# Kernel optimization log

Measured on AMD Instinct MI355X. Metric: run time of the kernel, lower is better.

Reference implementation:

```python
import jax, jax.numpy as jnp
import numpy as np

B, L, C, R = 2, 1024, 64, 32
RV, DQK, H, NSINK = 32, 64, 8, 4


def setup_inputs() -> dict:
    key = jax.random.key(0)
    ks = jax.random.split(key, 10)
    s_in = 1.0 / np.sqrt(C * R)
    s_r = 1.0 / np.sqrt(R)
    s_rv = 1.0 / np.sqrt(RV)
    return {
        "x": jax.random.normal(ks[0], (B, L, C, R), jnp.float32),
        "Wq": jax.random.normal(ks[1], (C * R, H * DQK), jnp.float32) * s_in,
        "bq": jax.random.normal(ks[2], (H * DQK,), jnp.float32) * s_in,
        "Wk": jax.random.normal(ks[3], (C * R, DQK), jnp.float32) * s_in,
        "bk": jax.random.normal(ks[4], (DQK,), jnp.float32) * s_in,
        "Wv": jax.random.normal(ks[5], (C, R, RV), jnp.float32) * s_r,
        "bv": jax.random.normal(ks[6], (C, RV), jnp.float32) * s_r,
        "Wo": jax.random.normal(ks[7], (C, RV, R), jnp.float32) * s_rv,
        "bo": jax.random.normal(ks[8], (C, R), jnp.float32) * s_rv,
        "sink_q": jax.random.normal(ks[9], (H, NSINK, DQK), jnp.float32),
    }


def reference(x, Wq, bq, Wk, bk, Wv, bv, Wo, bo, sink_q):
    b, l, c, r = x.shape
    h, d_qk = H, DQK
    scale = 1.0 / np.sqrt(d_qk)

    x_flat = x.reshape(b, l, c * r)
    q = (x_flat @ Wq + bq).reshape(b, l, h, d_qk)          # (B,L,H,D)
    k = x_flat @ Wk + bk                                    # (B,L,D) shared MQA key

    # fp32 softmax over time, as in the original
    logits = (jnp.einsum('blhd,bsd->bhls', q, k).astype(jnp.float32) * scale)
    attn = jax.nn.softmax(logits, axis=-1).astype(x.dtype)  # (B,H,L,S)

    # per-channel value projection (B,L,C,RV)
    v = jnp.einsum('blcr,cro->blco', x, Wv) + bv

    # AV with extra channel axis, fused with head-mean (same math as
    # einsum('bhls,bscv->bhlcv').mean(1))
    y = jnp.einsum('bhls,bscv->blcv', attn, v) / h          # (B,L,C,RV)

    # sink-query branch: learned queries attend over time, mean over (H, S)
    logits_s = (jnp.einsum('hsd,bld->bhsl', sink_q, k).astype(jnp.float32) * scale)
    attn_s = jax.nn.softmax(logits_s, axis=-1).astype(x.dtype)  # (B,H,S,L)
    y_sink = jnp.einsum('bhsl,blcv->bcv', attn_s, v) / (h * NSINK)
    y = y + y_sink[:, None]                                 # broadcast over L

    # per-channel output projection + residual
    y = jnp.einsum('blcv,cvr->blcr', y, Wo) + bo
    return x + y
```

## Files before the change

kernel.cpp:

```cpp
#include <hip/hip_runtime.h>
#include <hip/hip_bf16.h>
#include <math.h>


typedef __attribute__((ext_vector_type(8))) short short8;
typedef __attribute__((ext_vector_type(4))) short short4v;
typedef __attribute__((ext_vector_type(4))) float float4v;

__device__ __forceinline__ short f2b(float f) {
    __hip_bfloat16 h = __float2bfloat16(f);
    return __builtin_bit_cast(short, h);
}
__device__ __forceinline__ float b2f(short s) {
    unsigned u = ((unsigned)(unsigned short)s) << 16;
    return __builtin_bit_cast(float, u);
}

__global__ __launch_bounds__(256) void convert_w_kernel(
    const float* __restrict__ Wq, const float* __restrict__ Wk,
    short* __restrict__ Wt)
{
    const int n0 = blockIdx.x * 64;
    const int k0 = blockIdx.y * 64;
    const int tid = threadIdx.x;
    __shared__ float ts[64][65];
    for (int i = tid; i < 4096; i += 256) {
        int kk = i >> 6, nn = i & 63;
        int n = n0 + nn, k = k0 + kk;
        float v = (n < 512) ? Wq[(long)k * 512 + n] : Wk[(long)k * 64 + (n - 512)];
        ts[kk][nn] = v;
    }
    __syncthreads();
    for (int i = tid; i < 4096; i += 256) {
        int nn = i >> 6, kk = i & 63;
        Wt[(long)(n0 + nn) * 2048 + k0 + kk] = f2b(ts[kk][nn]);
    }
}

__global__ __launch_bounds__(256) void vproj_kernel(
    const float* __restrict__ x, const float* __restrict__ Wv,
    const float* __restrict__ bv, short* __restrict__ vt,
    short* __restrict__ xb)
{
    const int c = blockIdx.x;
    const int chunk = blockIdx.y;
    const int b = chunk >> 4;
    const int l0 = (chunk & 15) * 64;
    const int tid = threadIdx.x;
    __shared__ float Wc[32][33];
    __shared__ float xs[64][33];
    for (int i = tid; i < 1024; i += 256)
        Wc[i >> 5][i & 31] = Wv[(c * 32 + (i >> 5)) * 32 + (i & 31)];
    for (int i = tid; i < 2048; i += 256) {
        int s = i >> 5, r = i & 31;
        long gi = ((long)(b << 10) + l0 + s) * 2048 + c * 32 + r;
        float v = x[gi];
        xs[s][r] = v;
        xb[gi] = f2b(v);
    }
    __syncthreads();
    const int s = tid & 63;
    const int og = tid >> 6;
    #pragma unroll
    for (int oi = 0; oi < 8; ++oi) {
        int o = og * 8 + oi;
        float acc = bv[c * 32 + o];
        #pragma unroll
        for (int r = 0; r < 32; ++r) acc += xs[s][r] * Wc[r][o];
        vt[(long)b * (2048 * 1024) + (long)(c * 32 + o) * 1024 + l0 + s] = f2b(acc);
    }
}

__global__ __launch_bounds__(256) void qkproj_kernel(
    const short* __restrict__ xb, const short* __restrict__ Wt,
    float* __restrict__ qkpart)
{
    __shared__ short As[64][72];
    __shared__ short Bs[64][72];

    const int tid = threadIdx.x;
    const int wave = tid >> 6;
    const int lane = tid & 63;
    const int wm = wave >> 1, wn = wave & 1;
    const int m15 = lane & 15;
    const int quad = lane >> 4;
    const int row0 = blockIdx.y * 64;
    const int col0 = blockIdx.x * 64;
    const int kbase = blockIdx.z * 1024;
    float* outz = qkpart + (long)blockIdx.z * 1179648;

    float4v acc[2][2];
    #pragma unroll
    for (int i = 0; i < 2; ++i)
        #pragma unroll
        for (int j = 0; j < 2; ++j)
            #pragma unroll
            for (int r = 0; r < 4; ++r) acc[i][j][r] = 0.f;

    for (int kt = 0; kt < 16; ++kt) {
        int k0 = kbase + kt * 64;
        #pragma unroll
        for (int p = 0; p < 2; ++p) {
            int i = tid + p * 256;
            int m = i >> 3, kq = i & 7;
            *reinterpret_cast<short8*>(&As[m][kq * 8]) =
                *reinterpret_cast<const short8*>(&xb[(long)(row0 + m) * 2048 + k0 + kq * 8]);
        }
        #pragma unroll
        for (int p = 0; p < 2; ++p) {
            int i = tid + p * 256;
            int n = i >> 3, kq = i & 7;
            *reinterpret_cast<short8*>(&Bs[n][kq * 8]) =
                *reinterpret_cast<const short8*>(&Wt[(long)(col0 + n) * 2048 + k0 + kq * 8]);
        }
        __syncthreads();
        #pragma unroll
        for (int ks = 0; ks < 2; ++ks) {
            short8 a[2], b[2];
            #pragma unroll
            for (int t = 0; t < 2; ++t) {
                a[t] = *reinterpret_cast<const short8*>(&As[wm * 32 + t * 16 + m15][ks * 32 + quad * 8]);
                b[t] = *reinterpret_cast<const short8*>(&Bs[wn * 32 + t * 16 + m15][ks * 32 + quad * 8]);
            }
            #pragma unroll
            for (int ti = 0; ti < 2; ++ti)
                #pragma unroll
                for (int tj = 0; tj < 2; ++tj)
                    acc[ti][tj] = __builtin_amdgcn_mfma_f32_16x16x32_bf16(
                        a[ti], b[tj], acc[ti][tj], 0, 0, 0);
        }
        __syncthreads();
    }

    #pragma unroll
    for (int ti = 0; ti < 2; ++ti)
        #pragma unroll
        for (int r = 0; r < 4; ++r) {
            int row = row0 + wm * 32 + ti * 16 + quad * 4 + r;
            #pragma unroll
            for (int tj = 0; tj < 2; ++tj) {
                int col = col0 + wn * 32 + tj * 16 + m15;
                outz[(long)row * 576 + col] = acc[ti][tj][r];
            }
        }
}

__global__ __launch_bounds__(256) void convert_qk_kernel(
    const float* __restrict__ qkpart, const float* __restrict__ bq,
    const float* __restrict__ bk, short* __restrict__ qkb)
{
    int id = blockIdx.x * 256 + threadIdx.x;
    float4 a = reinterpret_cast<const float4*>(qkpart)[id];
    float4 b = reinterpret_cast<const float4*>(qkpart + 1179648)[id];
    int col4 = (id % 144) * 4;
    float4 bias = (col4 < 512)
        ? *reinterpret_cast<const float4*>(&bq[col4])
        : *reinterpret_cast<const float4*>(&bk[col4 - 512]);
    short4v o;
    o[0] = f2b(a.x + b.x + bias.x);
    o[1] = f2b(a.y + b.y + bias.y);
    o[2] = f2b(a.z + b.z + bias.z);
    o[3] = f2b(a.w + b.w + bias.w);
    reinterpret_cast<short4v*>(qkb)[id] = o;
}

__global__ __launch_bounds__(256) void qk_s_kernel(
    const short* __restrict__ qkb, short* __restrict__ S)
{
    const int s0 = blockIdx.x * 64;
    const int l0 = blockIdx.y * 64;
    const int b = blockIdx.z;
    const int tid = threadIdx.x;
    short* Sz = S + ((long)b << 23);

    __shared__ short Qs[64][520];
    __shared__ short Ks[64][72];

    #pragma unroll
    for (int p = 0; p < 16; ++p) {
        int i = tid + p * 256;
        int row = i >> 6, d8 = i & 63;
        *reinterpret_cast<short8*>(&Qs[row][d8 * 8]) =
            *reinterpret_cast<const short8*>(&qkb[(long)((b << 10) + l0 + row) * 576 + d8 * 8]);
    }
    #pragma unroll
    for (int p = 0; p < 2; ++p) {
        int i = tid + p * 256;
        int row = i >> 3, d8 = i & 7;
        *reinterpret_cast<short8*>(&Ks[row][d8 * 8]) =
            *reinterpret_cast<const short8*>(&qkb[(long)((b << 10) + s0 + row) * 576 + 512 + d8 * 8]);
    }
    __syncthreads();

    const int wave = tid >> 6;
    const int lane = tid & 63;
    const int wm = wave >> 1, wn = wave & 1;
    const int m15 = lane & 15;
    const int quad = lane >> 4;

    for (int h = 0; h < 8; ++h) {
        float4v acc[2][2];
        #pragma unroll
        for (int i = 0; i < 2; ++i)
            #pragma unroll
            for (int j = 0; j < 2; ++j)
                #pragma unroll
                for (int r = 0; r < 4; ++r) acc[i][j][r] = 0.f;

        #pragma unroll
        for (int ks = 0; ks < 2; ++ks) {
            short8 a[2], bfr[2];
            #pragma unroll
            for (int t = 0; t < 2; ++t) {
                a[t]   = *reinterpret_cast<const short8*>(
                    &Qs[wm * 32 + t * 16 + m15][h * 64 + ks * 32 + quad * 8]);
                bfr[t] = *reinterpret_cast<const short8*>(
                    &Ks[wn * 32 + t * 16 + m15][ks * 32 + quad * 8]);
            }
            #pragma unroll
            for (int ti = 0; ti < 2; ++ti)
                #pragma unroll
                for (int tj = 0; tj < 2; ++tj)
                    acc[ti][tj] = __builtin_amdgcn_mfma_f32_16x16x32_bf16(
                        a[ti], bfr[tj], acc[ti][tj], 0, 0, 0);
        }

        #pragma unroll
        for (int ti = 0; ti < 2; ++ti)
            #pragma unroll
            for (int r = 0; r < 4; ++r) {
                int l = l0 + wm * 32 + ti * 16 + quad * 4 + r;
                #pragma unroll
                for (int tj = 0; tj < 2; ++tj) {
                    int s = s0 + wn * 32 + tj * 16 + m15;
                    Sz[((long)h << 20) + (l << 10) + s] = f2b(acc[ti][tj][r] * 0.125f);
                }
            }
    }
}

__global__ __launch_bounds__(256) void softmax_avg_kernel(
    const short* __restrict__ S, short* __restrict__ P)
{
    const int l = blockIdx.x;
    const int b = blockIdx.y;
    const int tid = threadIdx.x;
    const int h = tid >> 5, j = tid & 31;
    const short* Sz = S + ((long)b << 23);

    __shared__ float es[8][1032];
    __shared__ float invd[8];

    const short* row = &Sz[((long)h << 20) + (l << 10)];
    float vals[32];
    float pm = -1e30f;
    #pragma unroll
    for (int i = 0; i < 32; ++i) {
        float f = b2f(row[i * 32 + j]);
        vals[i] = f;
        pm = fmaxf(pm, f);
    }
    #pragma unroll
    for (int off = 16; off > 0; off >>= 1) pm = fmaxf(pm, __shfl_down(pm, off, 32));
    pm = __shfl(pm, 0, 32);

    float ps = 0.f;
    #pragma unroll
    for (int i = 0; i < 32; ++i) {
        float e = __expf(vals[i] - pm);
        vals[i] = e;
        ps += e;
    }
    #pragma unroll
    for (int off = 16; off > 0; off >>= 1) ps += __shfl_down(ps, off, 32);
    if (j == 0) invd[h] = 1.f / (8.f * ps);
    __syncthreads();

    const float w = invd[h];
    #pragma unroll
    for (int i = 0; i < 32; ++i) es[h][i * 32 + j] = vals[i] * w;
    __syncthreads();

    for (int s = tid; s < 1024; s += 256) {
        float p = 0.f;
        #pragma unroll
        for (int hh = 0; hh < 8; ++hh) p += es[hh][s];
        P[((long)b << 20) + (l << 10) + s] = f2b(p);
    }
}

__global__ __launch_bounds__(256) void sink_kernel(
    const float* __restrict__ sink_q, const short* __restrict__ qkb,
    float* __restrict__ Psink)
{
    const int z = blockIdx.x;
    const int b = z >> 5;
    const int idx = z & 31;
    const int tid = threadIdx.x;

    __shared__ float sq[64];
    __shared__ float lgl[1024];
    __shared__ float red[4];
    __shared__ float mxs, invs;

    if (tid < 64) sq[tid] = sink_q[idx * 64 + tid];
    __syncthreads();

    float lmax = -1e30f;
    for (int l = tid; l < 1024; l += 256) {
        const short* kp = &qkb[(long)((b << 10) + l) * 576 + 512];
        float acc = 0.f;
        #pragma unroll
        for (int d8 = 0; d8 < 8; ++d8) {
            short8 kv = *reinterpret_cast<const short8*>(&kp[d8 * 8]);
            #pragma unroll
            for (int j = 0; j < 8; ++j) acc += b2f(kv[j]) * sq[d8 * 8 + j];
        }
        acc *= 0.125f;
        lgl[l] = acc;
        lmax = fmaxf(lmax, acc);
    }
    #pragma unroll
    for (int off = 32; off > 0; off >>= 1) lmax = fmaxf(lmax, __shfl_down(lmax, off, 64));
    if ((tid & 63) == 0) red[tid >> 6] = lmax;
    __syncthreads();
    if (tid == 0) mxs = fmaxf(fmaxf(red[0], red[1]), fmaxf(red[2], red[3]));
    __syncthreads();

    const float m = mxs;
    float psum = 0.f;
    for (int l = tid; l < 1024; l += 256) {
        float e = __expf(lgl[l] - m);
        lgl[l] = e;
        psum += e;
    }
    #pragma unroll
    for (int off = 32; off > 0; off >>= 1) psum += __shfl_down(psum, off, 64);
    if ((tid & 63) == 0) red[tid >> 6] = psum;
    __syncthreads();
    if (tid == 0) invs = 1.f / (red[0] + red[1] + red[2] + red[3]);
    __syncthreads();

    const float wgt = invs * (1.f / 32.f);
    for (int l = tid; l < 1024; l += 256)
        atomicAdd(&Psink[(b << 10) + l], lgl[l] * wgt);
}

__global__ __launch_bounds__(256) void sinky_kernel(
    const float* __restrict__ Psink, const short* __restrict__ vt,
    float* __restrict__ Ysink)
{
    const int b = blockIdx.y;
    const int tid = threadIdx.x;
    __shared__ float ps[1024];
    {
        float4 v = reinterpret_cast<const float4*>(&Psink[b << 10])[tid];
        *reinterpret_cast<float4*>(&ps[tid * 4]) = v;
    }
    __syncthreads();
    const int wave = tid >> 6;
    const int lane = tid & 63;
    const int co = blockIdx.x * 4 + wave;
    const short* vp = &vt[((long)b * 2048 + co) * 1024];
    float acc = 0.f;
    #pragma unroll
    for (int t = 0; t < 16; ++t) {
        int l = t * 64 + lane;
        acc += ps[l] * b2f(vp[l]);
    }
    #pragma unroll
    for (int off = 32; off > 0; off >>= 1) acc += __shfl_down(acc, off, 64);
    if (lane == 0) Ysink[(b << 11) + co] = acc;
}

__global__ __launch_bounds__(256) void y_fused_kernel(
    const short* __restrict__ P, const short* __restrict__ vt,
    const float* __restrict__ Ysink, const float* __restrict__ Wo,
    const float* __restrict__ bo, const float* __restrict__ x,
    float* __restrict__ out)
{
    __shared__ short As[128][72];
    __shared__ short Bs[64][72];

    const int tid = threadIdx.x;
    const int b = blockIdx.z;
    const int col0 = blockIdx.x * 64;
    const int row0 = blockIdx.y * 128;
    const short* Pz = P + ((long)b << 20);
    const short* Vz = vt + ((long)b * 2048 * 1024);

    const int wave = tid >> 6;
    const int lane = tid & 63;
    const int wm = wave >> 1, wn = wave & 1;
    const int m15 = lane & 15;
    const int quad = lane >> 4;

    float4v acc[4][2];
    #pragma unroll
    for (int i = 0; i < 4; ++i)
        #pragma unroll
        for (int j = 0; j < 2; ++j)
            #pragma unroll
            for (int r = 0; r < 4; ++r) acc[i][j][r] = 0.f;

    for (int kt = 0; kt < 16; ++kt) {
        int k0 = kt * 64;
        #pragma unroll
        for (int p = 0; p < 4; ++p) {
            int i = tid + p * 256;
            int m = i >> 3, kq = i & 7;
            *reinterpret_cast<short8*>(&As[m][kq * 8]) =
                *reinterpret_cast<const short8*>(&Pz[(long)(row0 + m) * 1024 + k0 + kq * 8]);
        }
        #pragma unroll
        for (int p = 0; p < 2; ++p) {
            int i = tid + p * 256;
            int n = i >> 3, kq = i & 7;
            *reinterpret_cast<short8*>(&Bs[n][kq * 8]) =
                *reinterpret_cast<const short8*>(&Vz[(long)(col0 + n) * 1024 + k0 + kq * 8]);
        }
        __syncthreads();
        #pragma unroll
        for (int ks = 0; ks < 2; ++ks) {
            short8 a[4], bb[2];
            #pragma unroll
            for (int t = 0; t < 4; ++t)
                a[t] = *reinterpret_cast<const short8*>(&As[wm * 64 + t * 16 + m15][ks * 32 + quad * 8]);
            #pragma unroll
            for (int t = 0; t < 2; ++t)
                bb[t] = *reinterpret_cast<const short8*>(&Bs[wn * 32 + t * 16 + m15][ks * 32 + quad * 8]);
            #pragma unroll
            for (int ti = 0; ti < 4; ++ti)
                #pragma unroll
                for (int tj = 0; tj < 2; ++tj)
                    acc[ti][tj] = __builtin_amdgcn_mfma_f32_16x16x32_bf16(
                        a[ti], bb[tj], acc[ti][tj], 0, 0, 0);
        }
        __syncthreads();
    }

    float ysv[2];
    #pragma unroll
    for (int tj = 0; tj < 2; ++tj)
        ysv[tj] = Ysink[(b << 11) + col0 + wn * 32 + tj * 16 + m15];

    #pragma unroll
    for (int ti = 0; ti < 4; ++ti)
        #pragma unroll
        for (int r = 0; r < 4; ++r) {
            int row = wm * 64 + ti * 16 + quad * 4 + r;
            #pragma unroll
            for (int tj = 0; tj < 2; ++tj) {
                int col = wn * 32 + tj * 16 + m15;
                As[row][col] = f2b(acc[ti][tj][r] + ysv[tj]);
            }
        }
    const int c0 = col0 >> 5;
    for (int i = tid; i < 4096; i += 256) {
        int n = i >> 6, k = i & 63;
        short v = 0;
        if ((n >> 5) == (k >> 5))
            v = f2b(Wo[((long)(c0 + (n >> 5)) * 32 + (k & 31)) * 32 + (n & 31)]);
        Bs[n][k] = v;
    }
    __syncthreads();

    float4v acc2[4][2];
    #pragma unroll
    for (int i = 0; i < 4; ++i)
        #pragma unroll
        for (int j = 0; j < 2; ++j)
            #pragma unroll
            for (int r = 0; r < 4; ++r) acc2[i][j][r] = 0.f;

    #pragma unroll
    for (int ks = 0; ks < 2; ++ks) {
        short8 a[4], bb[2];
        #pragma unroll
        for (int t = 0; t < 4; ++t)
            a[t] = *reinterpret_cast<const short8*>(&As[wm * 64 + t * 16 + m15][ks * 32 + quad * 8]);
        #pragma unroll
        for (int t = 0; t < 2; ++t)
            bb[t] = *reinterpret_cast<const short8*>(&Bs[wn * 32 + t * 16 + m15][ks * 32 + quad * 8]);
        #pragma unroll
        for (int ti = 0; ti < 4; ++ti)
            #pragma unroll
            for (int tj = 0; tj < 2; ++tj)
                acc2[ti][tj] = __builtin_amdgcn_mfma_f32_16x16x32_bf16(
                    a[ti], bb[tj], acc2[ti][tj], 0, 0, 0);
    }

    float bov[2];
    #pragma unroll
    for (int tj = 0; tj < 2; ++tj)
        bov[tj] = bo[col0 + wn * 32 + tj * 16 + m15];

    #pragma unroll
    for (int ti = 0; ti < 4; ++ti)
        #pragma unroll
        for (int r = 0; r < 4; ++r) {
            int row = (b << 10) + row0 + wm * 64 + ti * 16 + quad * 4 + r;
            #pragma unroll
            for (int tj = 0; tj < 2; ++tj) {
                int col = col0 + wn * 32 + tj * 16 + m15;
                long oi = (long)row * 2048 + col;
                out[oi] = x[oi] + bov[tj] + acc2[ti][tj][r];
            }
        }
}

extern "C" void kernel_launch(void* const* d_in, const int* in_sizes, int n_in,
                              void* d_out, int out_size, void* d_ws, size_t ws_size,
                              hipStream_t stream)
{
    const float* x  = (const float*)d_in[0];
    const float* Wq = (const float*)d_in[1];
    const float* bq = (const float*)d_in[2];
    const float* Wk = (const float*)d_in[3];
    const float* bk = (const float*)d_in[4];
    const float* Wv = (const float*)d_in[5];
    const float* bv = (const float*)d_in[6];
    const float* Wo = (const float*)d_in[7];
    const float* bo = (const float*)d_in[8];
    const float* sq = (const float*)d_in[9];
    float* out = (float*)d_out;

    float* ws = (float*)d_ws;
    float* qkpart = ws;
    short* qkb    = (short*)(ws + 2359296);
    short* P      = (short*)(ws + 2949120);
    float* Psink  = ws + 3997696;
    short* vt     = (short*)(ws + 3999744);
    float* Ysink  = ws + 6096896;
    float* region = ws + 6100992;
    short* xb     = (short*)region;
    short* Wt     = (short*)(region + 2097152);
    short* Sb     = (short*)region;

    dim3 blk(256);

    convert_w_kernel<<<dim3(9, 32), blk, 0, stream>>>(Wq, Wk, Wt);
    vproj_kernel<<<dim3(64, 32), blk, 0, stream>>>(x, Wv, bv, vt, xb);
    qkproj_kernel<<<dim3(9, 32, 2), blk, 0, stream>>>(xb, Wt, qkpart);
    convert_qk_kernel<<<dim3(1152), blk, 0, stream>>>(qkpart, bq, bk, qkb);
    qk_s_kernel<<<dim3(16, 16, 2), blk, 0, stream>>>(qkb, Sb);
    softmax_avg_kernel<<<dim3(1024, 2), blk, 0, stream>>>(Sb, P);
    hipMemsetAsync(Psink, 0, 2048 * sizeof(float), stream);
    sink_kernel<<<dim3(64), blk, 0, stream>>>(sq, qkb, Psink);
    sinky_kernel<<<dim3(512, 2), blk, 0, stream>>>(Psink, vt, Ysink);
    y_fused_kernel<<<dim3(32, 8, 2), blk, 0, stream>>>(
        P, vt, Ysink, Wo, bo, x, out);
}
```

Baseline: 194.2 us.

## Coalesce score stores, vectorize softmax, widen output GEMM tile with block-diagonal Wo

qk_s now loads one head of Q at a time into a small LDS tile and stages each 64x64 score tile through LDS so it can be written to global memory with 16-byte vector stores instead of scattered 2-byte ones. The softmax reads its rows with short8 vector loads, writes to LDS with float4 stores into a padded layout, and writes P with short4 stores. y_fused moves to 512 threads and 128-column tiles, and its output projection now does only the per-channel diagonal 32x32 block instead of multiplying by a mostly-zero 64x64 block. These target memory-transaction inefficiency and wasted MFMA work, at the cost of more barriers per head in qk_s and more register and LDS pressure in the larger y_fused block.

```diff
diff --git a/kernel.cpp b/kernel.cpp
--- a/kernel.cpp
+++ b/kernel.cpp
@@ -173,16 +173,10 @@
     const int tid = threadIdx.x;
     short* Sz = S + ((long)b << 23);
 
-    __shared__ short Qs[64][520];
+    __shared__ short Qh[64][72];
     __shared__ short Ks[64][72];
-
-    #pragma unroll
-    for (int p = 0; p < 16; ++p) {
-        int i = tid + p * 256;
-        int row = i >> 6, d8 = i & 63;
-        *reinterpret_cast<short8*>(&Qs[row][d8 * 8]) =
-            *reinterpret_cast<const short8*>(&qkb[(long)((b << 10) + l0 + row) * 576 + d8 * 8]);
-    }
+    __shared__ short Rp[64][72];
+
     #pragma unroll
     for (int p = 0; p < 2; ++p) {
         int i = tid + p * 256;
@@ -190,7 +184,6 @@
         *reinterpret_cast<short8*>(&Ks[row][d8 * 8]) =
             *reinterpret_cast<const short8*>(&qkb[(long)((b << 10) + s0 + row) * 576 + 512 + d8 * 8]);
     }
-    __syncthreads();
 
     const int wave = tid >> 6;
     const int lane = tid & 63;
@@ -199,6 +192,15 @@
     const int quad = lane >> 4;
 
     for (int h = 0; h < 8; ++h) {
+        #pragma unroll
+        for (int p = 0; p < 2; ++p) {
+            int i = tid + p * 256;
+            int row = i >> 3, d8 = i & 7;
+            *reinterpret_cast<short8*>(&Qh[row][d8 * 8]) =
+                *reinterpret_cast<const short8*>(&qkb[(long)((b << 10) + l0 + row) * 576 + h * 64 + d8 * 8]);
+        }
+        __syncthreads();
+
         float4v acc[2][2];
         #pragma unroll
         for (int i = 0; i < 2; ++i)
@@ -212,10 +214,8 @@
             short8 a[2], bfr[2];
             #pragma unroll
             for (int t = 0; t < 2; ++t) {
-                a[t]   = *reinterpret_cast<const short8*>(
-                    &Qs[wm * 32 + t * 16 + m15][h * 64 + ks * 32 + quad * 8]);
-                bfr[t] = *reinterpret_cast<const short8*>(
-                    &Ks[wn * 32 + t * 16 + m15][ks * 32 + quad * 8]);
+                a[t]   = *reinterpret_cast<const short8*>(&Qh[wm * 32 + t * 16 + m15][ks * 32 + quad * 8]);
+                bfr[t] = *reinterpret_cast<const short8*>(&Ks[wn * 32 + t * 16 + m15][ks * 32 + quad * 8]);
             }
             #pragma unroll
             for (int ti = 0; ti < 2; ++ti)
@@ -229,13 +229,19 @@
         for (int ti = 0; ti < 2; ++ti)
             #pragma unroll
             for (int r = 0; r < 4; ++r) {
-                int l = l0 + wm * 32 + ti * 16 + quad * 4 + r;
+                int row = wm * 32 + ti * 16 + quad * 4 + r;
                 #pragma unroll
-                for (int tj = 0; tj < 2; ++tj) {
-                    int s = s0 + wn * 32 + tj * 16 + m15;
-                    Sz[((long)h << 20) + (l << 10) + s] = f2b(acc[ti][tj][r] * 0.125f);
-                }
+                for (int tj = 0; tj < 2; ++tj)
+                    Rp[row][wn * 32 + tj * 16 + m15] = f2b(acc[ti][tj][r] * 0.125f);
             }
+        __syncthreads();
+        #pragma unroll
+        for (int p = 0; p < 2; ++p) {
+            int i = tid + p * 256;
+            int row = i >> 3, c8 = i & 7;
+            *reinterpret_cast<short8*>(&Sz[((long)h << 20) + ((long)(l0 + row) << 10) + s0 + c8 * 8]) =
+                *reinterpret_cast<const short8*>(&Rp[row][c8 * 8]);
+        }
     }
 }
 
@@ -248,17 +254,21 @@
     const int h = tid >> 5, j = tid & 31;
     const short* Sz = S + ((long)b << 23);
 
-    __shared__ float es[8][1032];
+    __shared__ float es[8][1056];
     __shared__ float invd[8];
 
-    const short* row = &Sz[((long)h << 20) + (l << 10)];
-    float vals[32];
+    const short* row = &Sz[((long)h << 20) + ((long)l << 10)];
+    float vals[4][8];
     float pm = -1e30f;
     #pragma unroll
-    for (int i = 0; i < 32; ++i) {
-        float f = b2f(row[i * 32 + j]);
-        vals[i] = f;
-        pm = fmaxf(pm, f);
+    for (int i = 0; i < 4; ++i) {
+        short8 v = *reinterpret_cast<const short8*>(&row[i * 256 + j * 8]);
+        #pragma unroll
+        for (int t = 0; t < 8; ++t) {
+            float f = b2f(v[t]);
+            vals[i][t] = f;
+            pm = fmaxf(pm, f);
+        }
     }
     #pragma unroll
     for (int off = 16; off > 0; off >>= 1) pm = fmaxf(pm, __shfl_down(pm, off, 32));
@@ -266,11 +276,13 @@
 
     float ps = 0.f;
     #pragma unroll
-    for (int i = 0; i < 32; ++i) {
-        float e = __expf(vals[i] - pm);
-        vals[i] = e;
-        ps += e;
-    }
+    for (int i = 0; i < 4; ++i)
+        #pragma unroll
+        for (int t = 0; t < 8; ++t) {
+            float e = __expf(vals[i][t] - pm);
+            vals[i][t] = e;
+            ps += e;
+        }
     #pragma unroll
     for (int off = 16; off > 0; off >>= 1) ps += __shfl_down(ps, off, 32);
     if (j == 0) invd[h] = 1.f / (8.f * ps);
@@ -278,14 +290,29 @@
 
     const float w = invd[h];
     #pragma unroll
-    for (int i = 0; i < 32; ++i) es[h][i * 32 + j] = vals[i] * w;
-    __syncthreads();
-
-    for (int s = tid; s < 1024; s += 256) {
-        float p = 0.f;
-        #pragma unroll
-        for (int hh = 0; hh < 8; ++hh) p += es[hh][s];
-        P[((long)b << 20) + (l << 10) + s] = f2b(p);
+    for (int i = 0; i < 4; ++i) {
+        int s = i * 256 + j * 8;
+        int s33 = s + (s >> 5);
+        float4 a = {vals[i][0] * w, vals[i][1] * w, vals[i][2] * w, vals[i][3] * w};
+        float4 c = {vals[i][4] * w, vals[i][5] * w, vals[i][6] * w, vals[i][7] * w};
+        *reinterpret_cast<float4*>(&es[h][s33]) = a;
+        *reinterpret_cast<float4*>(&es[h][s33 + 4]) = c;
+    }
+    __syncthreads();
+
+    {
+        int s = tid * 4;
+        short4v o;
+        #pragma unroll
+        for (int t = 0; t < 4; ++t) {
+            int st = s + t;
+            int s33 = st + (st >> 5);
+            float p = 0.f;
+            #pragma unroll
+            for (int hh = 0; hh < 8; ++hh) p += es[hh][s33];
+            o[t] = f2b(p);
+        }
+        *reinterpret_cast<short4v*>(&P[((long)b << 20) + ((long)l << 10) + s]) = o;
     }
 }
 
@@ -373,25 +400,27 @@
     if (lane == 0) Ysink[(b << 11) + co] = acc;
 }
 
-__global__ __launch_bounds__(256) void y_fused_kernel(
+__global__ __launch_bounds__(512) void y_fused_kernel(
     const short* __restrict__ P, const short* __restrict__ vt,
     const float* __restrict__ Ysink, const float* __restrict__ Wo,
     const float* __restrict__ bo, const float* __restrict__ x,
     float* __restrict__ out)
 {
-    __shared__ short As[128][72];
-    __shared__ short Bs[64][72];
+    __shared__ union SmU {
+        struct { short As[128][72]; short Bs[128][72]; } g;
+        struct { short Yt[128][136]; short WoLt[4][32][36]; } e;
+    } sm;
 
     const int tid = threadIdx.x;
     const int b = blockIdx.z;
-    const int col0 = blockIdx.x * 64;
+    const int col0 = blockIdx.x * 128;
     const int row0 = blockIdx.y * 128;
     const short* Pz = P + ((long)b << 20);
     const short* Vz = vt + ((long)b * 2048 * 1024);
 
     const int wave = tid >> 6;
     const int lane = tid & 63;
-    const int wm = wave >> 1, wn = wave & 1;
+    const int wm = wave >> 2, wn = wave & 3;
     const int m15 = lane & 15;
     const int quad = lane >> 4;
 
@@ -406,17 +435,17 @@
     for (int kt = 0; kt < 16; ++kt) {
         int k0 = kt * 64;
         #pragma unroll
-        for (int p = 0; p < 4; ++p) {
-            int i = tid + p * 256;
+        for (int p = 0; p < 2; ++p) {
+            int i = tid + p * 512;
             int m = i >> 3, kq = i & 7;
-            *reinterpret_cast<short8*>(&As[m][kq * 8]) =
+            *reinterpret_cast<short8*>(&sm.g.As[m][kq * 8]) =
                 *reinterpret_cast<const short8*>(&Pz[(long)(row0 + m) * 1024 + k0 + kq * 8]);
         }
         #pragma unroll
         for (int p = 0; p < 2; ++p) {
-            int i = tid + p * 256;
+            int i = tid + p * 512;
             int n = i >> 3, kq = i & 7;
-            *reinterpret_cast<short8*>(&Bs[n][kq * 8]) =
+            *reinterpret_cast<short8*>(&sm.g.Bs[n][kq * 8]) =
                 *reinterpret_cast<const short8*>(&Vz[(long)(col0 + n) * 1024 + k0 + kq * 8]);
         }
         __syncthreads();
@@ -425,10 +454,10 @@
             short8 a[4], bb[2];
             #pragma unroll
             for (int t = 0; t < 4; ++t)
-                a[t] = *reinterpret_cast<const short8*>(&As[wm * 64 + t * 16 + m15][ks * 32 + quad * 8]);
+                a[t] = *reinterpret_cast<const short8*>(&sm.g.As[wm * 64 + t * 16 + m15][ks * 32 + quad * 8]);
             #pragma unroll
             for (int t = 0; t < 2; ++t)
-                bb[t] = *reinterpret_cast<const short8*>(&Bs[wn * 32 + t * 16 + m15][ks * 32 + quad * 8]);
+                bb[t] = *reinterpret_cast<const short8*>(&sm.g.Bs[wn * 32 + t * 16 + m15][ks * 32 + quad * 8]);
             #pragma unroll
             for (int ti = 0; ti < 4; ++ti)
                 #pragma unroll
@@ -439,10 +468,13 @@
         __syncthreads();
     }
 
-    float ysv[2];
-    #pragma unroll
-    for (int tj = 0; tj < 2; ++tj)
-        ysv[tj] = Ysink[(b << 11) + col0 + wn * 32 + tj * 16 + m15];
+    float ysv[2], bov[2];
+    #pragma unroll
+    for (int tj = 0; tj < 2; ++tj) {
+        int col = col0 + wn * 32 + tj * 16 + m15;
+        ysv[tj] = Ysink[(b << 11) + col];
+        bov[tj] = bo[col];
+    }
 
     #pragma unroll
     for (int ti = 0; ti < 4; ++ti)
@@ -450,18 +482,13 @@
         for (int r = 0; r < 4; ++r) {
             int row = wm * 64 + ti * 16 + quad * 4 + r;
             #pragma unroll
-            for (int tj = 0; tj < 2; ++tj) {
-                int col = wn * 32 + tj * 16 + m15;
-                As[row][col] = f2b(acc[ti][tj][r] + ysv[tj]);
-            }
+            for (int tj = 0; tj < 2; ++tj)
+                sm.e.Yt[row][wn * 32 + tj * 16 + m15] = f2b(acc[ti][tj][r] + ysv[tj]);
         }
     const int c0 = col0 >> 5;
-    for (int i = tid; i < 4096; i += 256) {
-        int n = i >> 6, k = i & 63;
-        short v = 0;
-        if ((n >> 5) == (k >> 5))
-            v = f2b(Wo[((long)(c0 + (n >> 5)) * 32 + (k & 31)) * 32 + (n & 31)]);
-        Bs[n][k] = v;
+    for (int i = tid; i < 4096; i += 512) {
+        int c = i >> 10, o = (i >> 5) & 31, r = i & 31;
+        sm.e.WoLt[c][r][o] = f2b(Wo[((long)(c0 + c) * 32 + o) * 32 + r]);
     }
     __syncthreads();
 
@@ -473,15 +500,14 @@
             #pragma unroll
             for (int r = 0; r < 4; ++r) acc2[i][j][r] = 0.f;
 
-    #pragma unroll
-    for (int ks = 0; ks < 2; ++ks) {
+    {
         short8 a[4], bb[2];
         #pragma unroll
         for (int t = 0; t < 4; ++t)
-            a[t] = *reinterpret_cast<const short8*>(&As[wm * 64 + t * 16 + m15][ks * 32 + quad * 8]);
+            a[t] = *reinterpret_cast<const short8*>(&sm.e.Yt[wm * 64 + t * 16 + m15][wn * 32 + quad * 8]);
         #pragma unroll
         for (int t = 0; t < 2; ++t)
-            bb[t] = *reinterpret_cast<const short8*>(&Bs[wn * 32 + t * 16 + m15][ks * 32 + quad * 8]);
+            bb[t] = *reinterpret_cast<const short8*>(&sm.e.WoLt[wn][t * 16 + m15][quad * 8]);
         #pragma unroll
         for (int ti = 0; ti < 4; ++ti)
             #pragma unroll
@@ -489,11 +515,6 @@
                 acc2[ti][tj] = __builtin_amdgcn_mfma_f32_16x16x32_bf16(
                     a[ti], bb[tj], acc2[ti][tj], 0, 0, 0);
     }
-
-    float bov[2];
-    #pragma unroll
-    for (int tj = 0; tj < 2; ++tj)
-        bov[tj] = bo[col0 + wn * 32 + tj * 16 + m15];
 
     #pragma unroll
     for (int ti = 0; ti < 4; ++ti)
@@ -548,6 +569,6 @@
     hipMemsetAsync(Psink, 0, 2048 * sizeof(float), stream);
     sink_kernel<<<dim3(64), blk, 0, stream>>>(sq, qkb, Psink);
     sinky_kernel<<<dim3(512, 2), blk, 0, stream>>>(Psink, vt, Ysink);
-    y_fused_kernel<<<dim3(32, 8, 2), blk, 0, stream>>>(
+    y_fused_kernel<<<dim3(16, 8, 2), dim3(512), 0, stream>>>(
         P, vt, Ysink, Wo, bo, x, out);
 }
```

Measured after the change: 199.6 us. 1.03x slower.
